# Kernel optimization log

Measured on AMD Instinct MI355X. Metric: run time of the kernel, lower is better.

## Reference

```python
import jax, jax.numpy as jnp
import numpy as np

B, S, H, D = 16, 1024, 32, 128
HIDDEN = H * D            # 4096
INTER = 11008
EPS = 1e-6
THETA = 10000.0
SCALING = D ** -0.5


def setup_inputs() -> dict:
    key = jax.random.key(0)
    ks = jax.random.split(key, 12)
    w = lambda k, shape: jax.random.normal(k, shape, dtype=jnp.float32) * 0.02
    return {
        "positions": jax.random.randint(ks[0], (B,), 0, S, dtype=jnp.int32),
        "hidden_states": jax.random.normal(ks[1], (B, HIDDEN), dtype=jnp.float32),
        "k_cache": jax.random.normal(ks[2], (B, S, H, D), dtype=jnp.float32),
        "v_cache": jax.random.normal(ks[3], (B, S, H, D), dtype=jnp.float32),
        "qkv_w": w(ks[4], (HIDDEN, 3 * HIDDEN)),
        "qkv_b": jnp.zeros((3 * HIDDEN,), dtype=jnp.float32),
        "o_w": w(ks[5], (HIDDEN, HIDDEN)),
        "o_b": jnp.zeros((HIDDEN,), dtype=jnp.float32),
        "gate_up_w": w(ks[6], (HIDDEN, 2 * INTER)),
        "down_w": w(ks[7], (INTER, HIDDEN)),
        "ln1_w": jnp.ones((HIDDEN,), dtype=jnp.float32),
        "ln2_w": jnp.ones((HIDDEN,), dtype=jnp.float32),
    }


def rms_norm(x, w):
    var = jnp.mean(x * x, axis=-1, keepdims=True)
    return x * jax.lax.rsqrt(var + EPS) * w


def rotate_half(x):
    x1, x2 = jnp.split(x, 2, axis=-1)
    return jnp.concatenate([-x2, x1], axis=-1)


def apply_rope(x, positions):
    # x: [B, H, D], positions: [B] (GPT-NeoX style rotation)
    inv_freq = 1.0 / (THETA ** (jnp.arange(0, D, 2, dtype=jnp.float32) / D))  # [D/2]
    ang = positions.astype(jnp.float32)[:, None] * inv_freq                    # [B, D/2]
    cos = jnp.concatenate([jnp.cos(ang), jnp.cos(ang)], axis=-1)[:, None, :]   # [B,1,D]
    sin = jnp.concatenate([jnp.sin(ang), jnp.sin(ang)], axis=-1)[:, None, :]
    return x * cos + rotate_half(x) * sin


def reference(positions, hidden_states, k_cache, v_cache, qkv_w, qkv_b,
              o_w, o_b, gate_up_w, down_w, ln1_w, ln2_w):
    residual = hidden_states
    x = rms_norm(hidden_states, ln1_w)

    # QKV projection
    qkv = x @ qkv_w + qkv_b                       # [B, 3*HIDDEN]
    q, k, v = jnp.split(qkv, 3, axis=-1)
    q = q.reshape(B, H, D)
    k = k.reshape(B, H, D)
    v = v.reshape(B, H, D)

    # Fused RoPE on new q, k (cache already holds rotated keys)
    q = apply_rope(q, positions)
    k = apply_rope(k, positions)

    # Paged-cache write: store new k, v at slot `positions[b]`
    b_idx = jnp.arange(B)
    k_cache = k_cache.at[b_idx, positions].set(k)
    v_cache = v_cache.at[b_idx, positions].set(v)

    # Decode attention over the cache, masked to valid context j <= positions[b]
    scores = jnp.einsum("bhd,bshd->bhs", q, k_cache) * SCALING  # [B,H,S]
    valid = (jnp.arange(S)[None, :] <= positions[:, None])[:, None, :]  # [B,1,S]
    scores = jnp.where(valid, scores, jnp.finfo(scores.dtype).min)
    attn = jax.nn.softmax(scores, axis=-1)
    out = jnp.einsum("bhs,bshd->bhd", attn, v_cache).reshape(B, HIDDEN)

    x = out @ o_w + o_b
    hidden = residual + x

    # SwiGLU MLP
    residual = hidden
    x = rms_norm(hidden, ln2_w)
    gate_up = x @ gate_up_w                       # [B, 2*INTER]
    gate, up = jnp.split(gate_up, 2, axis=-1)
    x = (jax.nn.silu(gate) * up) @ down_w
    return residual + x
```

## Files before the change

kernel.cpp:

```cpp
#include <hip/hip_runtime.h>
#include <cstdint>
#include <cmath>

#define B_    16
#define S_    1024
#define H_    32
#define D_    128
#define HID   4096
#define INTER 11008
#define NC    8
#define CHUNK 128

__global__ __launch_bounds__(256) void rmsnorm_kernel(
    const float* __restrict__ in, const float* __restrict__ w, float* __restrict__ out)
{
    int b = blockIdx.x;
    int t = threadIdx.x;
    const float4* row = reinterpret_cast<const float4*>(in + (size_t)b * HID);
    float s = 0.f;
    for (int i = t; i < HID / 4; i += 256) {
        float4 v = row[i];
        s += v.x * v.x + v.y * v.y + v.z * v.z + v.w * v.w;
    }
    for (int off = 32; off; off >>= 1) s += __shfl_down(s, off, 64);
    __shared__ float red[4];
    int wid = t >> 6, lane = t & 63;
    if (lane == 0) red[wid] = s;
    __syncthreads();
    float tot = red[0] + red[1] + red[2] + red[3];
    float rstd = rsqrtf(tot / (float)HID + 1e-6f);
    const float4* wv4 = reinterpret_cast<const float4*>(w);
    float4* o4 = reinterpret_cast<float4*>(out + (size_t)b * HID);
    for (int i = t; i < HID / 4; i += 256) {
        float4 x = row[i], wv = wv4[i];
        float4 r;
        r.x = x.x * rstd * wv.x;
        r.y = x.y * rstd * wv.y;
        r.z = x.z * rstd * wv.z;
        r.w = x.w * rstd * wv.w;
        o4[i] = r;
    }
}

__global__ __launch_bounds__(256) void gemm16_splitk2(
    const float* __restrict__ x, const float* __restrict__ w,
    float* __restrict__ part, int K, int N, int kchunk)
{
    int j0 = (blockIdx.x * 256 + threadIdx.x) * 2;
    int k0 = blockIdx.y * kchunk;
    int k1 = k0 + kchunk;
    float2 acc[B_];
#pragma unroll
    for (int b = 0; b < B_; ++b) acc[b] = make_float2(0.f, 0.f);

    const float* wp = w + (size_t)k0 * N + j0;
    for (int k = k0; k < k1; k += 8) {
        float2 wv[8];
#pragma unroll
        for (int i = 0; i < 8; ++i)
            wv[i] = *reinterpret_cast<const float2*>(wp + (size_t)i * N);
        wp += 8 * (size_t)N;
#pragma unroll
        for (int b = 0; b < B_; ++b) {
            const float* xb = x + (size_t)b * K + k;
#pragma unroll
            for (int i = 0; i < 8; ++i) {
                float xv = xb[i];
                acc[b].x = fmaf(xv, wv[i].x, acc[b].x);
                acc[b].y = fmaf(xv, wv[i].y, acc[b].y);
            }
        }
    }
    float* pp = part + (size_t)blockIdx.y * B_ * N + j0;
#pragma unroll
    for (int b = 0; b < B_; ++b)
        *reinterpret_cast<float2*>(pp + (size_t)b * N) = acc[b];
}

__global__ __launch_bounds__(256) void reduce_bias_res(
    const float* __restrict__ part, int nsplit, int N,
    const float* __restrict__ bias, const float* __restrict__ res,
    float* __restrict__ out, int total)
{
    int i = blockIdx.x * 256 + threadIdx.x;
    if (i >= total) return;
    float s = 0.f;
    for (int p = 0; p < nsplit; ++p) s += part[(size_t)p * total + i];
    int jc = i % N;
    if (bias) s += bias[jc];
    if (res)  s += res[i];
    out[i] = s;
}

__global__ __launch_bounds__(256) void qkv_reduce_rope(
    const float* __restrict__ part, int nsplit, const float* __restrict__ bias,
    const int* __restrict__ positions,
    float* __restrict__ q_rot, float* __restrict__ k_rot, float* __restrict__ v_cp)
{
    int b = blockIdx.y;
    int t = threadIdx.x;
    int col = blockIdx.x * 256 + t;
    const int total = B_ * 3 * HID;
    size_t idx = (size_t)b * (3 * HID) + col;
    float s = 0.f;
    for (int p = 0; p < nsplit; ++p) s += part[(size_t)p * total + idx];
    s += bias[col];
    __shared__ float ls[256];
    ls[t] = s;
    __syncthreads();
    int region = col >> 12;
    float outv;
    if (region < 2) {
        int d = col & 127;
        float partner = ls[t ^ 64];
        float pos = (float)positions[b];
        float freq = powf(10000.0f, -(float)(d & 63) / 64.0f);
        float sv, cv;
        sincosf(pos * freq, &sv, &cv);
        outv = (d < 64) ? (s * cv - partner * sv) : (s * cv + partner * sv);
    } else {
        outv = s;
    }
    float* dst = (region == 0) ? q_rot : (region == 1) ? k_rot : v_cp;
    dst[(size_t)b * HID + (col & 4095)] = outv;
}

__global__ __launch_bounds__(256) void reduce_silu(
    const float* __restrict__ part, int nsplit, float* __restrict__ act)
{
    int i = blockIdx.x * 256 + threadIdx.x;
    if (i >= B_ * INTER) return;
    int b = i / INTER;
    int jc = i - b * INTER;
    size_t off = (size_t)b * (2 * INTER) + jc;
    float g = 0.f, u = 0.f;
    for (int p = 0; p < nsplit; ++p) {
        const float* pp = part + (size_t)p * B_ * 2 * INTER;
        g += pp[off];
        u += pp[off + INTER];
    }
    float sg = g / (1.f + expf(-g));
    act[i] = sg * u;
}

__global__ __launch_bounds__(128) void attn_split(
    const float* __restrict__ kc, const float* __restrict__ vc,
    const float* __restrict__ q_rot, const float* __restrict__ k_rot,
    const float* __restrict__ v_cp, const int* __restrict__ positions,
    float* __restrict__ pacc, float* __restrict__ pm, float* __restrict__ pl)
{
    int h = blockIdx.x, b = blockIdx.y, c = blockIdx.z, t = threadIdx.x;
    int pos = positions[b];
    int L = pos + 1;
    int j0c = c * CHUNK;
    size_t pidx = (((size_t)b * H_ + h) * NC + c);
    if (j0c >= L) {
        if (t == 0) { pm[pidx] = -INFINITY; pl[pidx] = 0.f; }
        pacc[pidx * D_ + t] = 0.f;
        return;
    }
    int jend = min(L, j0c + CHUNK);

    __shared__ float qs[D_];
    __shared__ float ks[32 * 132];
    __shared__ float vs[32 * D_];
    __shared__ float sc[32];
    qs[t] = q_rot[((size_t)b * H_ + h) * D_ + t];

    float m = -INFINITY, l = 0.f, acc = 0.f;
    const float scaling = 0.08838834764831845f;

    for (int j0 = j0c; j0 < jend; j0 += 32) {
        int nj = min(32, jend - j0);
        __syncthreads();
        for (int idx = t; idx < 32 * 32; idx += 128) {
            int r = idx >> 5, c4 = idx & 31;
            int jj = j0 + r;
            float4 kvv = make_float4(0.f, 0.f, 0.f, 0.f);
            float4 vvv = kvv;
            if (jj < jend) {
                if (jj == pos) {
                    kvv = reinterpret_cast<const float4*>(k_rot + ((size_t)b * H_ + h) * D_)[c4];
                    vvv = reinterpret_cast<const float4*>(v_cp  + ((size_t)b * H_ + h) * D_)[c4];
                } else {
                    kvv = reinterpret_cast<const float4*>(kc + (((size_t)b * S_ + jj) * H_ + h) * D_)[c4];
                    vvv = reinterpret_cast<const float4*>(vc + (((size_t)b * S_ + jj) * H_ + h) * D_)[c4];
                }
            }
            *reinterpret_cast<float4*>(&ks[r * 132 + c4 * 4]) = kvv;
            *reinterpret_cast<float4*>(&vs[r * D_  + c4 * 4]) = vvv;
        }
        __syncthreads();
        {
            int jr = t >> 2, q4 = t & 3;
            const float* kr = ks + jr * 132 + q4 * 32;
            const float* qq = qs + q4 * 32;
            float s = 0.f;
#pragma unroll
            for (int cc = 0; cc < 32; ++cc) s = fmaf(qq[cc], kr[cc], s);
            s += __shfl_xor(s, 1, 64);
            s += __shfl_xor(s, 2, 64);
            if (q4 == 0) sc[jr] = s * scaling;
        }
        __syncthreads();
        float p[32];
        float mt = m;
#pragma unroll
        for (int r = 0; r < 32; ++r) {
            float v = (r < nj) ? sc[r] : -INFINITY;
            p[r] = v;
            mt = fmaxf(mt, v);
        }
        float scale = expf(m - mt);
        float ps = 0.f;
#pragma unroll
        for (int r = 0; r < 32; ++r) {
            float e = (r < nj) ? expf(p[r] - mt) : 0.f;
            p[r] = e;
            ps += e;
        }
        m = mt;
        l = l * scale + ps;
        acc *= scale;
#pragma unroll
        for (int r = 0; r < 32; ++r) acc = fmaf(p[r], vs[r * D_ + t], acc);
    }
    pm[pidx] = m;
    pl[pidx] = l;
    pacc[pidx * D_ + t] = acc;
}

__global__ __launch_bounds__(128) void attn_combine(
    const float* __restrict__ pacc, const float* __restrict__ pm,
    const float* __restrict__ pl, float* __restrict__ out)
{
    int h = blockIdx.x, b = blockIdx.y, t = threadIdx.x;
    size_t base = ((size_t)b * H_ + h) * NC;
    float M = -INFINITY;
#pragma unroll
    for (int c = 0; c < NC; ++c) M = fmaxf(M, pm[base + c]);
    float l = 0.f, a = 0.f;
#pragma unroll
    for (int c = 0; c < NC; ++c) {
        float w = expf(pm[base + c] - M);
        l = fmaf(pl[base + c], w, l);
        a = fmaf(pacc[(base + c) * D_ + t], w, a);
    }
    out[((size_t)b * H_ + h) * D_ + t] = a / l;
}

extern "C" void kernel_launch(void* const* d_in, const int* in_sizes, int n_in,
                              void* d_out, int out_size, void* d_ws, size_t ws_size,
                              hipStream_t stream)
{
    const int*   positions = (const int*)  d_in[0];
    const float* hidden    = (const float*)d_in[1];
    const float* kc        = (const float*)d_in[2];
    const float* vc        = (const float*)d_in[3];
    const float* qkv_w     = (const float*)d_in[4];
    const float* qkv_b     = (const float*)d_in[5];
    const float* o_w       = (const float*)d_in[6];
    const float* o_b       = (const float*)d_in[7];
    const float* gu_w      = (const float*)d_in[8];
    const float* down_w    = (const float*)d_in[9];
    const float* ln1       = (const float*)d_in[10];
    const float* ln2       = (const float*)d_in[11];
    float* out = (float*)d_out;
    float* ws  = (float*)d_ws;

    float* x1      = ws;
    float* q_rot   = x1 + (size_t)B_ * HID;
    float* k_rot   = q_rot + (size_t)B_ * HID;
    float* v_cp    = k_rot + (size_t)B_ * HID;
    float* attn_o  = v_cp + (size_t)B_ * HID;
    float* hidden2 = attn_o + (size_t)B_ * HID;
    float* x2      = hidden2 + (size_t)B_ * HID;
    float* act     = x2 + (size_t)B_ * HID;
    float* part    = act + (size_t)B_ * INTER;

    float* pacc = part;
    float* pm   = pacc + (size_t)B_ * H_ * NC * D_;
    float* pl   = pm + (size_t)B_ * H_ * NC;

    rmsnorm_kernel<<<B_, 256, 0, stream>>>(hidden, ln1, x1);
    gemm16_splitk2<<<dim3(24, 32), 256, 0, stream>>>(x1, qkv_w, part, HID, 3 * HID, 128);
    qkv_reduce_rope<<<dim3(48, B_), 256, 0, stream>>>(part, 32, qkv_b, positions,
                                                      q_rot, k_rot, v_cp);
    attn_split<<<dim3(H_, B_, NC), 128, 0, stream>>>(kc, vc, q_rot, k_rot, v_cp, positions,
                                                     pacc, pm, pl);
    attn_combine<<<dim3(H_, B_), 128, 0, stream>>>(pacc, pm, pl, attn_o);
    gemm16_splitk2<<<dim3(8, 64), 256, 0, stream>>>(attn_o, o_w, part, HID, HID, 64);
    reduce_bias_res<<<256, 256, 0, stream>>>(part, 64, HID, o_b, hidden, hidden2, B_ * HID);
    rmsnorm_kernel<<<B_, 256, 0, stream>>>(hidden2, ln2, x2);
    gemm16_splitk2<<<dim3(43, 16), 256, 0, stream>>>(x2, gu_w, part, HID, 2 * INTER, 256);
    reduce_silu<<<688, 256, 0, stream>>>(part, 16, act);
    gemm16_splitk2<<<dim3(8, 43), 256, 0, stream>>>(act, down_w, part, INTER, HID, 256);
    reduce_bias_res<<<256, 256, 0, stream>>>(part, 43, HID, nullptr, hidden2, out, B_ * HID);
}
```

Measured before the change: 343.9 us.

## Stream V directly from global in attention and rebalance down-proj split-K

The attention split kernel no longer stages V tiles in shared memory. Each thread reads its V column straight from global memory during accumulation, and the query is held in registers with an interleaved access pattern into the K tile. The GEMM is templated on its unroll depth, and the down projection now uses a 64-way split with unroll 4, which suits chunks of 172. The aim is less shared-memory traffic and better occupancy in attention, plus more blocks for the down GEMM, at the cost of more reduction partials and possibly less latency hiding on the V loads.

```diff
diff --git a/kernel.cpp b/kernel.cpp
--- a/kernel.cpp
+++ b/kernel.cpp
@@ -42,6 +42,7 @@
     }
 }
 
+template <int UNR>
 __global__ __launch_bounds__(256) void gemm16_splitk2(
     const float* __restrict__ x, const float* __restrict__ w,
     float* __restrict__ part, int K, int N, int kchunk)
@@ -54,17 +55,17 @@
     for (int b = 0; b < B_; ++b) acc[b] = make_float2(0.f, 0.f);
 
     const float* wp = w + (size_t)k0 * N + j0;
-    for (int k = k0; k < k1; k += 8) {
-        float2 wv[8];
-#pragma unroll
-        for (int i = 0; i < 8; ++i)
+    for (int k = k0; k < k1; k += UNR) {
+        float2 wv[UNR];
+#pragma unroll
+        for (int i = 0; i < UNR; ++i)
             wv[i] = *reinterpret_cast<const float2*>(wp + (size_t)i * N);
-        wp += 8 * (size_t)N;
+        wp += (size_t)UNR * N;
 #pragma unroll
         for (int b = 0; b < B_; ++b) {
             const float* xb = x + (size_t)b * K + k;
 #pragma unroll
-            for (int i = 0; i < 8; ++i) {
+            for (int i = 0; i < UNR; ++i) {
                 float xv = xb[i];
                 acc[b].x = fmaf(xv, wv[i].x, acc[b].x);
                 acc[b].y = fmaf(xv, wv[i].y, acc[b].y);
@@ -160,12 +161,15 @@
         return;
     }
     int jend = min(L, j0c + CHUNK);
-
-    __shared__ float qs[D_];
+    int jr = t >> 2, q4 = t & 3;
+
     __shared__ float ks[32 * 132];
-    __shared__ float vs[32 * D_];
     __shared__ float sc[32];
-    qs[t] = q_rot[((size_t)b * H_ + h) * D_ + t];
+
+    size_t bh = ((size_t)b * H_ + h) * D_;
+    float qq[32];
+#pragma unroll
+    for (int ci = 0; ci < 32; ++ci) qq[ci] = q_rot[bh + q4 + 4 * ci];
 
     float m = -INFINITY, l = 0.f, acc = 0.f;
     const float scaling = 0.08838834764831845f;
@@ -177,27 +181,18 @@
             int r = idx >> 5, c4 = idx & 31;
             int jj = j0 + r;
             float4 kvv = make_float4(0.f, 0.f, 0.f, 0.f);
-            float4 vvv = kvv;
-            if (jj < jend) {
-                if (jj == pos) {
-                    kvv = reinterpret_cast<const float4*>(k_rot + ((size_t)b * H_ + h) * D_)[c4];
-                    vvv = reinterpret_cast<const float4*>(v_cp  + ((size_t)b * H_ + h) * D_)[c4];
-                } else {
-                    kvv = reinterpret_cast<const float4*>(kc + (((size_t)b * S_ + jj) * H_ + h) * D_)[c4];
-                    vvv = reinterpret_cast<const float4*>(vc + (((size_t)b * S_ + jj) * H_ + h) * D_)[c4];
-                }
-            }
+            if (jj < jend)
+                kvv = (jj == pos)
+                    ? reinterpret_cast<const float4*>(k_rot + bh)[c4]
+                    : reinterpret_cast<const float4*>(kc + (((size_t)b * S_ + jj) * H_ + h) * D_)[c4];
             *reinterpret_cast<float4*>(&ks[r * 132 + c4 * 4]) = kvv;
-            *reinterpret_cast<float4*>(&vs[r * D_  + c4 * 4]) = vvv;
         }
         __syncthreads();
         {
-            int jr = t >> 2, q4 = t & 3;
-            const float* kr = ks + jr * 132 + q4 * 32;
-            const float* qq = qs + q4 * 32;
+            const float* kr = ks + jr * 132 + q4;
             float s = 0.f;
 #pragma unroll
-            for (int cc = 0; cc < 32; ++cc) s = fmaf(qq[cc], kr[cc], s);
+            for (int ci = 0; ci < 32; ++ci) s = fmaf(qq[ci], kr[4 * ci], s);
             s += __shfl_xor(s, 1, 64);
             s += __shfl_xor(s, 2, 64);
             if (q4 == 0) sc[jr] = s * scaling;
@@ -223,7 +218,15 @@
         l = l * scale + ps;
         acc *= scale;
 #pragma unroll
-        for (int r = 0; r < 32; ++r) acc = fmaf(p[r], vs[r * D_ + t], acc);
+        for (int r = 0; r < 32; ++r) {
+            if (r < nj) {
+                int jj = j0 + r;
+                float v = (jj == pos)
+                    ? v_cp[bh + t]
+                    : vc[(((size_t)b * S_ + jj) * H_ + h) * D_ + t];
+                acc = fmaf(p[r], v, acc);
+            }
+        }
     }
     pm[pidx] = m;
     pl[pidx] = l;
@@ -283,17 +286,17 @@
     float* pl   = pm + (size_t)B_ * H_ * NC;
 
     rmsnorm_kernel<<<B_, 256, 0, stream>>>(hidden, ln1, x1);
-    gemm16_splitk2<<<dim3(24, 32), 256, 0, stream>>>(x1, qkv_w, part, HID, 3 * HID, 128);
+    gemm16_splitk2<8><<<dim3(24, 32), 256, 0, stream>>>(x1, qkv_w, part, HID, 3 * HID, 128);
     qkv_reduce_rope<<<dim3(48, B_), 256, 0, stream>>>(part, 32, qkv_b, positions,
                                                       q_rot, k_rot, v_cp);
     attn_split<<<dim3(H_, B_, NC), 128, 0, stream>>>(kc, vc, q_rot, k_rot, v_cp, positions,
                                                      pacc, pm, pl);
     attn_combine<<<dim3(H_, B_), 128, 0, stream>>>(pacc, pm, pl, attn_o);
-    gemm16_splitk2<<<dim3(8, 64), 256, 0, stream>>>(attn_o, o_w, part, HID, HID, 64);
+    gemm16_splitk2<8><<<dim3(8, 64), 256, 0, stream>>>(attn_o, o_w, part, HID, HID, 64);
     reduce_bias_res<<<256, 256, 0, stream>>>(part, 64, HID, o_b, hidden, hidden2, B_ * HID);
     rmsnorm_kernel<<<B_, 256, 0, stream>>>(hidden2, ln2, x2);
-    gemm16_splitk2<<<dim3(43, 16), 256, 0, stream>>>(x2, gu_w, part, HID, 2 * INTER, 256);
+    gemm16_splitk2<8><<<dim3(43, 16), 256, 0, stream>>>(x2, gu_w, part, HID, 2 * INTER, 256);
     reduce_silu<<<688, 256, 0, stream>>>(part, 16, act);
-    gemm16_splitk2<<<dim3(8, 43), 256, 0, stream>>>(act, down_w, part, INTER, HID, 256);
-    reduce_bias_res<<<256, 256, 0, stream>>>(part, 43, HID, nullptr, hidden2, out, B_ * HID);
-}
+    gemm16_splitk2<4><<<dim3(8, 64), 256, 0, stream>>>(act, down_w, part, INTER, HID, 172);
+    reduce_bias_res<<<256, 256, 0, stream>>>(part, 64, HID, nullptr, hidden2, out, B_ * HID);
+}
```

After: 408.4 us. 1.19x slower.
